# Optimization experiments

Measured on AMD Instinct MI355X. Metric: run time of the kernel, lower is better.

The kernel has to match this reference:

```python
import jax, jax.numpy as jnp
import numpy as np

IN_F, OUT_F, GROUP = 4096, 4096, 128
N_GROUPS = IN_F // GROUP
NIB_SHIFTS = jnp.arange(8, dtype=jnp.int32) * 4  # 8 nibbles per int32


def dequantize(qweight, qzeros, scales, g_idx):
    """GPTQ/exllama 4-bit grouped dequant -> fp16 weight [K, N]."""
    # unpack qweight: [K//8, N] int32 -> [K//8, 8, N] nibbles -> [K, N]
    w_q = (qweight[:, None, :] >> NIB_SHIFTS[None, :, None]) & 0xF
    w_q = w_q.reshape(-1, qweight.shape[1])  # [K, N]
    # unpack qzeros: [G, N//8] int32 -> [G, N//8, 8] -> [G, N]
    z_q = (qzeros[:, :, None] >> NIB_SHIFTS[None, None, :]) & 0xF
    z_q = z_q.reshape(qzeros.shape[0], -1)  # [G, N]
    # exllama stores zero-points minus one: w = (q - (z + 1)) * scale
    z_rows = z_q[g_idx]            # [K, N] int32
    s_rows = scales[g_idx]         # [K, N] fp16
    return (w_q - z_rows - 1).astype(jnp.float16) * s_rows


def setup_inputs() -> dict:
    key = jax.random.key(0)
    k_x, k_qw, k_qz, k_s, k_b = jax.random.split(key, 5)
    x = jax.random.normal(k_x, (4, 2048, IN_F), dtype=jnp.float16)
    qweight = jax.random.randint(k_qw, (IN_F // 8, OUT_F), 0, 2147483647, dtype=jnp.int32)
    qzeros = jax.random.randint(k_qz, (N_GROUPS, OUT_F // 8), 0, 2147483647, dtype=jnp.int32)
    scales = (jax.random.uniform(k_s, (N_GROUPS, OUT_F), dtype=jnp.float32) * 0.01 + 0.001).astype(jnp.float16)
    g_idx = (jnp.arange(IN_F, dtype=jnp.int32) // GROUP).astype(jnp.int32)
    bias = (jax.random.normal(k_b, (OUT_F,), dtype=jnp.float32) * 0.02).astype(jnp.float16)
    return {"x": x, "qweight": qweight, "qzeros": qzeros, "scales": scales, "g_idx": g_idx, "bias": bias}


def reference(x, qweight, qzeros, scales, g_idx, bias):
    W = dequantize(qweight, qzeros, scales, g_idx)      # [K, N] fp16
    lead = x.shape[:-1]
    out = jnp.dot(x.reshape(-1, x.shape[-1]), W)        # fp16 GEMM, [T, N]
    out = out + bias
    return out.reshape(lead + (W.shape[1],))
```

## Files before the change

### kernel.cpp

```cpp
#include <hip/hip_runtime.h>
#include <hip/hip_bf16.h>
#include <stdint.h>

#define M_TOT 8192
#define N_TOT 4096
#define K_TOT 4096
#define GROUP 128


using f32x4  = __attribute__((ext_vector_type(4))) float;
using bf16x8 = __attribute__((ext_vector_type(8))) __bf16;

typedef __attribute__((address_space(3))) void as3_void;
typedef const __attribute__((address_space(1))) void as1_void;

__global__ __launch_bounds__(256) void prep(
    const float* __restrict__ x,
    const int*   __restrict__ qweight,
    const int*   __restrict__ qzeros,
    const float* __restrict__ scales,
    const int*   __restrict__ g_idx,
    __bf16* __restrict__ xb,
    __bf16* __restrict__ Wt)
{
    const int tid = threadIdx.x;
    if (blockIdx.x < 4096) {
        __shared__ __align__(16) unsigned short T[64 * 72];
        const int k0 = (blockIdx.x & 63) * 64;
        const int n0 = (blockIdx.x >> 6) * 64;
        const int g  = g_idx[k0];

        #pragma unroll
        for (int i = 0; i < 2; ++i) {
            const int idx = tid + i * 256;
            const int r   = idx >> 6;
            const int n   = idx & 63;
            const int qi  = qweight[(size_t)((k0 >> 3) + r) * N_TOT + n0 + n];
            const int zi  = qzeros[g * (N_TOT / 8) + ((n0 + n) >> 3)];
            const float s = scales[g * N_TOT + n0 + n];
            const float zs = (float)(((zi >> ((n & 7) * 4)) & 0xF) + 1) * s;
            bf16x8 v;
            #pragma unroll
            for (int j = 0; j < 8; ++j)
                v[j] = (__bf16)((float)((qi >> (4 * j)) & 0xF) * s - zs);
            *(bf16x8*)&T[n * 72 + r * 8] = v;
        }
        __syncthreads();

        const int n = tid >> 2;
        const int c = (tid & 3) * 16;
        const bf16x8 a = *(const bf16x8*)&T[n * 72 + c];
        const bf16x8 b = *(const bf16x8*)&T[n * 72 + c + 8];
        __bf16* dst = Wt + (size_t)(n0 + n) * K_TOT + k0 + c;
        *(bf16x8*)dst = a;
        *(bf16x8*)(dst + 8) = b;
    } else {
        const size_t t = (size_t)(blockIdx.x - 4096) * 256 + tid;
        const float4 f0 = *(const float4*)(x + t * 8);
        const float4 f1 = *(const float4*)(x + t * 8 + 4);
        bf16x8 v;
        v[0]=(__bf16)f0.x; v[1]=(__bf16)f0.y; v[2]=(__bf16)f0.z; v[3]=(__bf16)f0.w;
        v[4]=(__bf16)f1.x; v[5]=(__bf16)f1.y; v[6]=(__bf16)f1.z; v[7]=(__bf16)f1.w;
        *(bf16x8*)(xb + t * 8) = v;
    }
}

#define GBM 256
#define GBN 256
#define GBK 64
#define NKT (K_TOT / GBK)

#define BAR() do { asm volatile("" ::: "memory"); \
                   __builtin_amdgcn_s_barrier();  \
                   asm volatile("" ::: "memory"); } while (0)
#define WAIT_LGKM0() asm volatile("s_waitcnt lgkmcnt(0)" ::: "memory")
#define WAIT_VM8()   asm volatile("s_waitcnt vmcnt(8)"   ::: "memory")
#define WAIT_VM0()   asm volatile("s_waitcnt vmcnt(0)"   ::: "memory")

#define GPHASE(q, STAGE_STMT, TAIL_STMT)                                      \
    {                                                                         \
        bf16x8 av[2][2];                                                      \
        _Pragma("unroll")                                                     \
        for (int ks = 0; ks < 2; ++ks) {                                      \
            av[0][ks] = ldfrag(&Abuf[qa][0], wm, 2 * (q), ks);                \
            av[1][ks] = ldfrag(&Abuf[qa][0], wm, 2 * (q) + 1, ks);            \
        }                                                                     \
        STAGE_STMT;                                                           \
        BAR();                                                                \
        WAIT_LGKM0();                                                         \
        __builtin_amdgcn_s_setprio(1);                                        \
        _Pragma("unroll")                                                     \
        for (int ks = 0; ks < 2; ++ks)                                        \
            _Pragma("unroll")                                                 \
            for (int mtl = 0; mtl < 2; ++mtl)                                 \
                _Pragma("unroll")                                             \
                for (int nt = 0; nt < 4; ++nt)                                \
                    acc[2 * (q) + mtl][nt] =                                  \
                        __builtin_amdgcn_mfma_f32_16x16x32_bf16(              \
                            av[mtl][ks], bv[nt][ks], acc[2 * (q) + mtl][nt],  \
                            0, 0, 0);                                         \
        __builtin_amdgcn_s_setprio(0);                                        \
        TAIL_STMT;                                                            \
        BAR();                                                                \
    }

__global__ __launch_bounds__(512, 2) void gemm8p(
    const __bf16* __restrict__ xb,
    const __bf16* __restrict__ Wt,
    const float*  __restrict__ bias,
    float* __restrict__ out)
{
    __shared__ __align__(16) unsigned short Abuf[3][GBM * GBK];
    __shared__ __align__(16) unsigned short Bbuf[2][GBM * GBK];

    const int tid  = threadIdx.x;
    const int wid  = tid >> 6;
    const int lane = tid & 63;
    const int l15  = lane & 15;
    const int quad = lane >> 4;

    int bid = blockIdx.x;
    bid = (bid & 7) * (512 >> 3) + (bid >> 3);
    const int tn = bid & (N_TOT / GBN - 1);
    const int tm = bid >> 4;
    const int m0 = tm * GBM;
    const int n0 = tn * GBN;

    const int wm = (wid >> 2) * 128;
    const int wn = (wid & 3) * 64;

    f32x4 acc[8][4];
    #pragma unroll
    for (int i = 0; i < 8; ++i)
        #pragma unroll
        for (int j = 0; j < 4; ++j)
            acc[i][j] = (f32x4)0.f;

    auto stage = [&](unsigned short* ldsb, int h,
                     const __bf16* __restrict__ base, int row0, int kt) {
        #pragma unroll
        for (int j = 0; j < 2; ++j) {
            const int c  = j * 512 + tid;
            const int rl = c >> 3;
            const int kc = (c & 7) ^ (rl & 7);
            const __bf16* ga = base + (size_t)(row0 + h * 128 + rl) * K_TOT
                             + kt * GBK + kc * 8;
            __builtin_amdgcn_global_load_lds((as1_void*)ga,
                (as3_void*)&ldsb[h * 8192 + (j * 512 + wid * 64) * 8],
                16, 0, 0);
        }
    };
    auto ldfrag = [&](const unsigned short* ldsb, int wbase, int mt,
                      int ks) -> bf16x8 {
        const int r = wbase + mt * 16 + l15;
        return *(const bf16x8*)
            &ldsb[r * GBK + (((ks * 4 + quad) ^ (r & 7)) << 3)];
    };

    stage(&Abuf[0][0], 0, xb, m0, 0); stage(&Abuf[0][0], 1, xb, m0, 0);
    stage(&Bbuf[0][0], 0, Wt, n0, 0); stage(&Bbuf[0][0], 1, Wt, n0, 0);
    stage(&Abuf[1][0], 0, xb, m0, 1); stage(&Abuf[1][0], 1, xb, m0, 1);
    stage(&Bbuf[1][0], 0, Wt, n0, 1); stage(&Bbuf[1][0], 1, Wt, n0, 1);
    WAIT_VM8();
    BAR();

    bf16x8 bv[4][2];

    int qa = 0;
    int qs = 2;
    int p  = 0;

    for (int t = 0; t < NKT; ++t) {
        {
            #pragma unroll
            for (int nt = 0; nt < 4; ++nt)
                #pragma unroll
                for (int ks = 0; ks < 2; ++ks)
                    bv[nt][ks] = ldfrag(&Bbuf[p][0], wn, nt, ks);
            bf16x8 av[2][2];
            #pragma unroll
            for (int ks = 0; ks < 2; ++ks) {
                av[0][ks] = ldfrag(&Abuf[qa][0], wm, 0, ks);
                av[1][ks] = ldfrag(&Abuf[qa][0], wm, 1, ks);
            }
            if (t + 2 < NKT) stage(&Abuf[qs][0], 0, xb, m0, t + 2);
            BAR();
            WAIT_LGKM0();
            __builtin_amdgcn_s_setprio(1);
            #pragma unroll
            for (int ks = 0; ks < 2; ++ks)
                #pragma unroll
                for (int mtl = 0; mtl < 2; ++mtl)
                    #pragma unroll
                    for (int nt = 0; nt < 4; ++nt)
                        acc[mtl][nt] = __builtin_amdgcn_mfma_f32_16x16x32_bf16(
                            av[mtl][ks], bv[nt][ks], acc[mtl][nt], 0, 0, 0);
            __builtin_amdgcn_s_setprio(0);
            BAR();
        }
        GPHASE(1, if (t + 2 < NKT) stage(&Abuf[qs][0], 1, xb, m0, t + 2), );
        GPHASE(2, if (t + 2 < NKT) stage(&Bbuf[p][0], 0, Wt, n0, t + 2), );
        GPHASE(3, if (t + 2 < NKT) stage(&Bbuf[p][0], 1, Wt, n0, t + 2),
               if (t < NKT - 2) { WAIT_VM8(); } else { WAIT_VM0(); });

        qa = (qa == 2) ? 0 : qa + 1;
        qs = (qs == 2) ? 0 : qs + 1;
        p ^= 1;
    }

    #pragma unroll
    for (int nt = 0; nt < 4; ++nt) {
        const int col = n0 + wn + nt * 16 + l15;
        const float bb = bias[col];
        #pragma unroll
        for (int mt = 0; mt < 8; ++mt) {
            const int rowb = m0 + wm + mt * 16 + quad * 4;
            #pragma unroll
            for (int i = 0; i < 4; ++i)
                out[(size_t)(rowb + i) * N_TOT + col] = acc[mt][nt][i] + bb;
        }
    }
}

#define FBM 256
#define FBN 128
#define FBKP 72

__global__ __launch_bounds__(256, 2) void gptq_gemm_fused(
    const float* __restrict__ x, const int* __restrict__ qweight,
    const int* __restrict__ qzeros, const float* __restrict__ scales,
    const int* __restrict__ g_idx, const float* __restrict__ bias,
    float* __restrict__ out)
{
    __shared__ __align__(16) unsigned short As[FBM * FBKP];
    __shared__ __align__(16) unsigned short Bt[FBN * FBKP];

    const int tid  = threadIdx.x;
    const int wave = tid >> 6;
    const int lane = tid & 63;
    const int n0 = blockIdx.x * FBN;
    const int m0 = blockIdx.y * FBM;
    const int wm = (wave >> 1) * 64;
    const int wn = (wave & 1) * 64;
    const int l15  = lane & 15;
    const int quad = lane >> 4;

    f32x4 acc[2][4][4];
    #pragma unroll
    for (int mi = 0; mi < 2; ++mi)
        #pragma unroll
        for (int i = 0; i < 4; ++i)
            #pragma unroll
            for (int j = 0; j < 4; ++j)
                acc[mi][i][j] = (f32x4)0.f;

    const int nb  = tid & 31;
    const int r   = tid >> 5;
    const int zsh = (nb & 7) * 4;

    for (int kt = 0; kt < K_TOT / 64; ++kt) {
        const int k0 = kt * 64;
        #pragma unroll
        for (int i = 0; i < 8; ++i) {
            const int c   = tid + i * 256;
            const int row = c >> 3;
            const int cb  = (c & 7) << 3;
            const float* xp = x + (size_t)(m0 + row) * K_TOT + (k0 + cb);
            const float4 f0 = *(const float4*)xp;
            const float4 f1 = *(const float4*)(xp + 4);
            bf16x8 v;
            v[0]=(__bf16)f0.x; v[1]=(__bf16)f0.y; v[2]=(__bf16)f0.z; v[3]=(__bf16)f0.w;
            v[4]=(__bf16)f1.x; v[5]=(__bf16)f1.y; v[6]=(__bf16)f1.z; v[7]=(__bf16)f1.w;
            *(bf16x8*)&As[row * FBKP + cb] = v;
        }
        const int g    = g_idx[k0];
        const int qrow = (k0 >> 3) + r;
        #pragma unroll
        for (int dn = 0; dn < 4; ++dn) {
            const int n  = nb + dn * 32;
            const int qi = qweight[(size_t)qrow * N_TOT + (n0 + n)];
            const int zi = qzeros[g * (N_TOT / 8) + ((n0 + n) >> 3)];
            const float s = scales[g * N_TOT + (n0 + n)];
            const float zs = (float)(((zi >> zsh) & 0xF) + 1) * s;
            bf16x8 v;
            #pragma unroll
            for (int j = 0; j < 8; ++j)
                v[j] = (__bf16)((float)((qi >> (4 * j)) & 0xF) * s - zs);
            *(bf16x8*)&Bt[n * FBKP + r * 8] = v;
        }
        __syncthreads();
        #pragma unroll
        for (int ks = 0; ks < 2; ++ks) {
            bf16x8 bvv[4];
            #pragma unroll
            for (int nt = 0; nt < 4; ++nt)
                bvv[nt] = *(const bf16x8*)&Bt[(wn + nt * 16 + l15) * FBKP + ks * 32 + quad * 8];
            #pragma unroll
            for (int mi = 0; mi < 2; ++mi) {
                bf16x8 av[4];
                #pragma unroll
                for (int mt = 0; mt < 4; ++mt)
                    av[mt] = *(const bf16x8*)&As[(mi * 128 + wm + mt * 16 + l15) * FBKP + ks * 32 + quad * 8];
                #pragma unroll
                for (int mt = 0; mt < 4; ++mt)
                    #pragma unroll
                    for (int nt = 0; nt < 4; ++nt)
                        acc[mi][mt][nt] = __builtin_amdgcn_mfma_f32_16x16x32_bf16(
                            av[mt], bvv[nt], acc[mi][mt][nt], 0, 0, 0);
            }
        }
        __syncthreads();
    }
    #pragma unroll
    for (int mi = 0; mi < 2; ++mi)
        #pragma unroll
        for (int nt = 0; nt < 4; ++nt) {
            const int col = n0 + wn + nt * 16 + l15;
            const float bvv = bias[col];
            #pragma unroll
            for (int mt = 0; mt < 4; ++mt) {
                const int rowb = m0 + mi * 128 + wm + mt * 16 + quad * 4;
                #pragma unroll
                for (int i = 0; i < 4; ++i)
                    out[(size_t)(rowb + i) * N_TOT + col] = acc[mi][mt][nt][i] + bvv;
            }
        }
}

extern "C" void kernel_launch(void* const* d_in, const int* in_sizes, int n_in,
                              void* d_out, int out_size, void* d_ws, size_t ws_size,
                              hipStream_t stream) {
    const float* x  = (const float*)d_in[0];
    const int*   qw = (const int*)d_in[1];
    const int*   qz = (const int*)d_in[2];
    const float* sc = (const float*)d_in[3];
    const int*   gi = (const int*)d_in[4];
    const float* bs = (const float*)d_in[5];
    float* out = (float*)d_out;

    const size_t xb_bytes = (size_t)M_TOT * K_TOT * 2;
    const size_t wt_bytes = (size_t)N_TOT * K_TOT * 2;

    if (ws_size >= xb_bytes + wt_bytes) {
        __bf16* xb = (__bf16*)d_ws;
        __bf16* Wt = (__bf16*)((char*)d_ws + xb_bytes);
        const int cast_blocks = (M_TOT * K_TOT) / (256 * 8);
        prep<<<dim3(4096 + cast_blocks), dim3(256), 0, stream>>>(
            x, qw, qz, sc, gi, xb, Wt);
        gemm8p<<<dim3((M_TOT / GBM) * (N_TOT / GBN)), dim3(512), 0, stream>>>(
            xb, Wt, bs, out);
    } else {
        gptq_gemm_fused<<<dim3(N_TOT / FBN, M_TOT / FBM), dim3(256), 0, stream>>>(
            x, qw, qz, sc, gi, bs, out);
    }
}
```

Baseline: 490.4 us.

## Shrink A staging to double buffer and drop explicit LDS waits

```diff
diff --git a/kernel.cpp b/kernel.cpp
--- a/kernel.cpp
+++ b/kernel.cpp
@@ -56,8 +56,8 @@
         *(bf16x8*)(dst + 8) = b;
     } else {
         const size_t t = (size_t)(blockIdx.x - 4096) * 256 + tid;
-        const float4 f0 = *(const float4*)(x + t * 8);
-        const float4 f1 = *(const float4*)(x + t * 8 + 4);
+        const f32x4 f0 = __builtin_nontemporal_load((const f32x4*)(x + t * 8));
+        const f32x4 f1 = __builtin_nontemporal_load((const f32x4*)(x + t * 8) + 1);
         bf16x8 v;
         v[0]=(__bf16)f0.x; v[1]=(__bf16)f0.y; v[2]=(__bf16)f0.z; v[3]=(__bf16)f0.w;
         v[4]=(__bf16)f1.x; v[5]=(__bf16)f1.y; v[6]=(__bf16)f1.z; v[7]=(__bf16)f1.w;
@@ -73,8 +73,7 @@
 #define BAR() do { asm volatile("" ::: "memory"); \
                    __builtin_amdgcn_s_barrier();  \
                    asm volatile("" ::: "memory"); } while (0)
-#define WAIT_LGKM0() asm volatile("s_waitcnt lgkmcnt(0)" ::: "memory")
-#define WAIT_VM8()   asm volatile("s_waitcnt vmcnt(8)"   ::: "memory")
+#define WAIT_VM4()   asm volatile("s_waitcnt vmcnt(4)"   ::: "memory")
 #define WAIT_VM0()   asm volatile("s_waitcnt vmcnt(0)"   ::: "memory")
 
 #define GPHASE(q, STAGE_STMT, TAIL_STMT)                                      \
@@ -82,12 +81,11 @@
         bf16x8 av[2][2];                                                      \
         _Pragma("unroll")                                                     \
         for (int ks = 0; ks < 2; ++ks) {                                      \
-            av[0][ks] = ldfrag(&Abuf[qa][0], wm, 2 * (q), ks);                \
-            av[1][ks] = ldfrag(&Abuf[qa][0], wm, 2 * (q) + 1, ks);            \
+            av[0][ks] = ldfrag(&Abuf[buf][0], wm, 2 * (q), ks);               \
+            av[1][ks] = ldfrag(&Abuf[buf][0], wm, 2 * (q) + 1, ks);           \
         }                                                                     \
         STAGE_STMT;                                                           \
         BAR();                                                                \
-        WAIT_LGKM0();                                                         \
         __builtin_amdgcn_s_setprio(1);                                        \
         _Pragma("unroll")                                                     \
         for (int ks = 0; ks < 2; ++ks)                                        \
@@ -110,7 +108,7 @@
     const float*  __restrict__ bias,
     float* __restrict__ out)
 {
-    __shared__ __align__(16) unsigned short Abuf[3][GBM * GBK];
+    __shared__ __align__(16) unsigned short Abuf[2][GBM * GBK];
     __shared__ __align__(16) unsigned short Bbuf[2][GBM * GBK];
 
     const int tid  = threadIdx.x;
@@ -159,33 +157,29 @@
 
     stage(&Abuf[0][0], 0, xb, m0, 0); stage(&Abuf[0][0], 1, xb, m0, 0);
     stage(&Bbuf[0][0], 0, Wt, n0, 0); stage(&Bbuf[0][0], 1, Wt, n0, 0);
-    stage(&Abuf[1][0], 0, xb, m0, 1); stage(&Abuf[1][0], 1, xb, m0, 1);
     stage(&Bbuf[1][0], 0, Wt, n0, 1); stage(&Bbuf[1][0], 1, Wt, n0, 1);
-    WAIT_VM8();
+    WAIT_VM4();
     BAR();
 
     bf16x8 bv[4][2];
 
-    int qa = 0;
-    int qs = 2;
-    int p  = 0;
-
     for (int t = 0; t < NKT; ++t) {
+        const int buf = t & 1;
+
         {
             #pragma unroll
             for (int nt = 0; nt < 4; ++nt)
                 #pragma unroll
                 for (int ks = 0; ks < 2; ++ks)
-                    bv[nt][ks] = ldfrag(&Bbuf[p][0], wn, nt, ks);
+                    bv[nt][ks] = ldfrag(&Bbuf[buf][0], wn, nt, ks);
             bf16x8 av[2][2];
             #pragma unroll
             for (int ks = 0; ks < 2; ++ks) {
-                av[0][ks] = ldfrag(&Abuf[qa][0], wm, 0, ks);
-                av[1][ks] = ldfrag(&Abuf[qa][0], wm, 1, ks);
+                av[0][ks] = ldfrag(&Abuf[buf][0], wm, 0, ks);
+                av[1][ks] = ldfrag(&Abuf[buf][0], wm, 1, ks);
             }
-            if (t + 2 < NKT) stage(&Abuf[qs][0], 0, xb, m0, t + 2);
+            if (t + 1 < NKT) stage(&Abuf[buf ^ 1][0], 0, xb, m0, t + 1);
             BAR();
-            WAIT_LGKM0();
             __builtin_amdgcn_s_setprio(1);
             #pragma unroll
             for (int ks = 0; ks < 2; ++ks)
@@ -198,14 +192,10 @@
             __builtin_amdgcn_s_setprio(0);
             BAR();
         }
-        GPHASE(1, if (t + 2 < NKT) stage(&Abuf[qs][0], 1, xb, m0, t + 2), );
-        GPHASE(2, if (t + 2 < NKT) stage(&Bbuf[p][0], 0, Wt, n0, t + 2), );
-        GPHASE(3, if (t + 2 < NKT) stage(&Bbuf[p][0], 1, Wt, n0, t + 2),
-               if (t < NKT - 2) { WAIT_VM8(); } else { WAIT_VM0(); });
-
-        qa = (qa == 2) ? 0 : qa + 1;
-        qs = (qs == 2) ? 0 : qs + 1;
-        p ^= 1;
+        GPHASE(1, if (t + 1 < NKT) stage(&Abuf[buf ^ 1][0], 1, xb, m0, t + 1), );
+        GPHASE(2, if (t + 2 < NKT) stage(&Bbuf[buf][0], 0, Wt, n0, t + 2), );
+        GPHASE(3, if (t + 2 < NKT) stage(&Bbuf[buf][0], 1, Wt, n0, t + 2),
+               if (t < NKT - 2) { WAIT_VM4(); } else { WAIT_VM0(); });
     }
 
     #pragma unroll
```

Measured after the change: 472.5 us. 3.6% less time.
